# Optimization experiments

Measured on AMD Instinct MI355X. Metric: run time of the kernel, lower is better.

Reference implementation:

```python
import jax, jax.numpy as jnp
import numpy as np

B, D_IN, T = 8, 1024, 2048
CODEBOOK_SIZE, CODEBOOK_DIM = 8192, 8
EPS = 1e-12  # F.normalize default eps


def _l2_normalize(x, axis=-1):
    # matches torch F.normalize: x / max(||x||_2, eps)
    n = jnp.sqrt(jnp.sum(x * x, axis=axis, keepdims=True))
    return x / jnp.maximum(n, EPS)


def setup_inputs() -> dict:
    key = jax.random.key(0)
    k_z, k_wi, k_bi, k_wo, k_bo, k_cb = jax.random.split(key, 6)
    z = jax.random.normal(k_z, (B, D_IN, T), dtype=jnp.float32)
    # weight_norm(Conv1d) is a reparameterization; the effective weight is a
    # plain [out, in] matrix for a kernel_size=1 conv.
    w_in = jax.random.normal(k_wi, (CODEBOOK_DIM, D_IN), dtype=jnp.float32) * (1.0 / np.sqrt(D_IN))
    b_in = jax.random.normal(k_bi, (CODEBOOK_DIM,), dtype=jnp.float32) * 0.01
    w_out = jax.random.normal(k_wo, (D_IN, CODEBOOK_DIM), dtype=jnp.float32) * (1.0 / np.sqrt(CODEBOOK_DIM))
    b_out = jax.random.normal(k_bo, (D_IN,), dtype=jnp.float32) * 0.01
    codebook = jax.random.normal(k_cb, (CODEBOOK_SIZE, CODEBOOK_DIM), dtype=jnp.float32)
    return {"z": z, "w_in": w_in, "b_in": b_in, "w_out": w_out, "b_out": b_out, "codebook": codebook}


def reference(z, w_in, b_in, w_out, b_out, codebook):
    b, _, t = z.shape
    # in_project: 1x1 conv == matmul over channel dim
    z_e = jnp.einsum('od,bdt->bot', w_in, z) + b_in[None, :, None]  # [B, cd, T]

    # decode_latents
    enc = z_e.transpose(0, 2, 1).reshape(b * t, CODEBOOK_DIM)  # (b t) d
    enc_n = _l2_normalize(enc, axis=1)
    cb_n = _l2_normalize(codebook, axis=1)
    # dist = ||e||^2 - 2 e @ c^T + ||c||^2  (materializes [B*T, K] as original)
    dist = (jnp.sum(enc_n * enc_n, axis=1, keepdims=True)
            - 2.0 * (enc_n @ cb_n.T)
            + jnp.sum(cb_n * cb_n, axis=1)[None, :])
    indices = jnp.argmax(-dist, axis=1).reshape(b, t)  # [B, T] int
    # decode_code uses the UNnormalized codebook
    z_q = codebook[indices].transpose(0, 2, 1)  # [B, cd, T]

    # straight-through estimator
    z_q_st = z_e + jax.lax.stop_gradient(z_q - z_e)
    out = jnp.einsum('od,bdt->bot', w_out, z_q_st) + b_out[None, :, None]  # [B, D, T]

    commit_loss = jnp.zeros((b,), dtype=z.dtype)
    codebook_loss = jnp.zeros((b,), dtype=z.dtype)
    return (out, commit_loss, codebook_loss, indices, z_e)
```

## Files before the change

### kernel.cpp

```cpp
#include <hip/hip_runtime.h>
#include <math.h>

static constexpr int Bq  = 8;
static constexpr int DIN = 1024;
static constexpr int TTT = 2048;
static constexpr int KCB = 8192;

static constexpr int NCH = 64;
static constexpr int CPC = 128;

static constexpr size_t OUT_OFS  = 0;
static constexpr size_t LOSS_OFS = (size_t)Bq * DIN * TTT;
static constexpr size_t IDX_OFS  = LOSS_OFS + 16;
static constexpr size_t ZE_OFS   = IDX_OFS + (size_t)Bq * TTT;

static constexpr size_t WS_CBN  = 0;
static constexpr size_t WS_C2   = 65536;
static constexpr size_t WS_WT   = 73728;
static constexpr size_t WS_ENC  = 81920;
static constexpr size_t WS_PART = 212992;
static constexpr size_t WS_IDXI = WS_PART + (size_t)2 * NCH * 16384;

__global__ __launch_bounds__(256) void k0_prep(
    const float* __restrict__ w_in, const float* __restrict__ codebook,
    float* __restrict__ ws, float* __restrict__ out)
{
  int tid = blockIdx.x * 256 + threadIdx.x;
  if (tid < KCB) {
    const float4* cp = (const float4*)(codebook + (size_t)tid * 8);
    float4 a = cp[0], b = cp[1];
    float v[8] = {a.x, a.y, a.z, a.w, b.x, b.y, b.z, b.w};
    float n2 = 0.f;
#pragma unroll
    for (int o = 0; o < 8; o++) n2 = fmaf(v[o], v[o], n2);
    float dn = fmaxf(sqrtf(n2), 1e-12f);
    float u[8];
    float s2 = 0.f;
#pragma unroll
    for (int o = 0; o < 8; o++) { u[o] = v[o] / dn; s2 = fmaf(u[o], u[o], s2); }
    float4* wp = (float4*)(ws + WS_CBN + (size_t)tid * 8);
    wp[0] = make_float4(u[0], u[1], u[2], u[3]);
    wp[1] = make_float4(u[4], u[5], u[6], u[7]);
    ws[WS_C2 + tid] = 0.5f * s2;
  } else if (tid < KCB + DIN) {
    int d = tid - KCB;
#pragma unroll
    for (int o = 0; o < 8; o++) ws[WS_WT + (size_t)d * 8 + o] = w_in[(size_t)o * DIN + d];
  } else if (tid < KCB + DIN + 16) {
    out[LOSS_OFS + (tid - KCB - DIN)] = 0.f;
  }
}

__global__ __launch_bounds__(512) void k1_proj_in(
    const float* __restrict__ z, const float* __restrict__ b_in,
    float* __restrict__ ws, float* __restrict__ out)
{
  __shared__ __align__(16) float lds[16384];
  int tid = threadIdx.x;
  int bx = blockIdx.x;
  int b = bx >> 5;
  int t0 = (bx & 31) << 6;
  {
    const float4* src = (const float4*)(ws + WS_WT);
    float4* dst = (float4*)lds;
#pragma unroll
    for (int i = 0; i < 4; i++) dst[tid + 512 * i] = src[tid + 512 * i];
  }
  __syncthreads();
  int tt = tid & 15;
  int dg = tid >> 4;
  const float* zb = z + (size_t)b * DIN * TTT + t0 + (tt << 2);
  float4 acc[8];
#pragma unroll
  for (int o = 0; o < 8; o++) acc[o] = make_float4(0.f, 0.f, 0.f, 0.f);
  int dbase = dg << 5;
  const float4* wl = (const float4*)lds;
#pragma unroll 8
  for (int i = 0; i < 32; i++) {
    int d = dbase + i;
    float4 zv = *(const float4*)(zb + (size_t)d * TTT);
    float4 w0 = wl[d * 2 + 0];
    float4 w1 = wl[d * 2 + 1];
#define ACC1(o, wsc)                                    \
    acc[o].x = fmaf(wsc, zv.x, acc[o].x);               \
    acc[o].y = fmaf(wsc, zv.y, acc[o].y);               \
    acc[o].z = fmaf(wsc, zv.z, acc[o].z);               \
    acc[o].w = fmaf(wsc, zv.w, acc[o].w);
    ACC1(0, w0.x) ACC1(1, w0.y) ACC1(2, w0.z) ACC1(3, w0.w)
    ACC1(4, w1.x) ACC1(5, w1.y) ACC1(6, w1.z) ACC1(7, w1.w)
#undef ACC1
  }
  __syncthreads();
  {
    float4* pl = (float4*)lds;
#pragma unroll
    for (int o = 0; o < 8; o++) pl[dg * 128 + o * 16 + tt] = acc[o];
  }
  __syncthreads();
  int o = tid >> 6;
  int t = tid & 63;
  float s = 0.f;
#pragma unroll
  for (int g = 0; g < 32; g++) s += lds[g * 512 + o * 64 + t];
  s += b_in[o];
  out[ZE_OFS + ((size_t)b * 8 + o) * TTT + t0 + t] = s;
  ws[WS_ENC + ((size_t)(b * TTT + t0 + t)) * 8 + o] = s;
}

__global__ __launch_bounds__(256) void k2_scan(float* __restrict__ ws)
{
  __shared__ __align__(16) float4 scb[CPC * 2];
  __shared__ float sch[CPC];
  int tid = threadIdx.x;
  int rb = blockIdx.x >> 6;
  int ch = blockIdx.x & 63;
  int k0 = ch << 7;
  if (tid < CPC) {
    const float4* src = (const float4*)(ws + WS_CBN + (size_t)(k0 + tid) * 8);
    scb[tid * 2]     = src[0];
    scb[tid * 2 + 1] = src[1];
    sch[tid] = ws[WS_C2 + k0 + tid];
  }
  int rbase = (rb << 11) + tid;

#define DECL_ROW(j) float4 m##j##a, m##j##b; float b##j = 3.4e38f; int i##j = 0;
  DECL_ROW(0) DECL_ROW(1) DECL_ROW(2) DECL_ROW(3)
  DECL_ROW(4) DECL_ROW(5) DECL_ROW(6) DECL_ROW(7)
#undef DECL_ROW

#define LOAD_ROW(j) {                                                         \
    int r = rbase + (j << 8);                                                 \
    const float4* ep = (const float4*)(ws + WS_ENC + (size_t)r * 8);          \
    float4 a = ep[0], c = ep[1];                                              \
    float n2 = 0.f;                                                           \
    n2 = fmaf(a.x, a.x, n2); n2 = fmaf(a.y, a.y, n2);                         \
    n2 = fmaf(a.z, a.z, n2); n2 = fmaf(a.w, a.w, n2);                         \
    n2 = fmaf(c.x, c.x, n2); n2 = fmaf(c.y, c.y, n2);                         \
    n2 = fmaf(c.z, c.z, n2); n2 = fmaf(c.w, c.w, n2);                         \
    float dn = fmaxf(sqrtf(n2), 1e-12f);                                      \
    m##j##a.x = -(a.x / dn); m##j##a.y = -(a.y / dn);                         \
    m##j##a.z = -(a.z / dn); m##j##a.w = -(a.w / dn);                         \
    m##j##b.x = -(c.x / dn); m##j##b.y = -(c.y / dn);                         \
    m##j##b.z = -(c.z / dn); m##j##b.w = -(c.w / dn); }
  LOAD_ROW(0) LOAD_ROW(1) LOAD_ROW(2) LOAD_ROW(3)
  LOAD_ROW(4) LOAD_ROW(5) LOAD_ROW(6) LOAD_ROW(7)
#undef LOAD_ROW

  __syncthreads();
#pragma unroll 4
  for (int k = 0; k < CPC; k++) {
    float4 c0 = scb[2 * k];
    float4 c1 = scb[2 * k + 1];
    float cc = sch[k];
    int kk = k0 + k;
#define STEP(j) {                                                             \
    float s = cc;                                                             \
    s = fmaf(m##j##a.x, c0.x, s); s = fmaf(m##j##a.y, c0.y, s);               \
    s = fmaf(m##j##a.z, c0.z, s); s = fmaf(m##j##a.w, c0.w, s);               \
    s = fmaf(m##j##b.x, c1.x, s); s = fmaf(m##j##b.y, c1.y, s);               \
    s = fmaf(m##j##b.z, c1.z, s); s = fmaf(m##j##b.w, c1.w, s);               \
    if (s < b##j) { b##j = s; i##j = kk; } }
    STEP(0) STEP(1) STEP(2) STEP(3) STEP(4) STEP(5) STEP(6) STEP(7)
#undef STEP
  }
  float2* part = (float2*)(ws + WS_PART);
#define STORE_ROW(j) \
  part[(size_t)ch * 16384 + rbase + (j << 8)] = make_float2(b##j, __int_as_float(i##j));
  STORE_ROW(0) STORE_ROW(1) STORE_ROW(2) STORE_ROW(3)
  STORE_ROW(4) STORE_ROW(5) STORE_ROW(6) STORE_ROW(7)
#undef STORE_ROW
}

__global__ __launch_bounds__(256) void k2b_reduce(float* __restrict__ ws, float* __restrict__ out)
{
  int r = blockIdx.x * 256 + threadIdx.x;
  const float2* part = (const float2*)(ws + WS_PART);
  float best = 3.4e38f;
  int bi = 0;
#pragma unroll 8
  for (int ch = 0; ch < NCH; ch++) {
    float2 p = part[(size_t)ch * 16384 + r];
    if (p.x < best) { best = p.x; bi = __float_as_int(p.y); }
  }
  out[IDX_OFS + r] = (float)bi;
  ((int*)(ws + WS_IDXI))[r] = bi;
}

__global__ __launch_bounds__(256) void k3_proj_out(
    const float* __restrict__ codebook, const float* __restrict__ w_out,
    const float* __restrict__ b_out, const float* __restrict__ ws,
    float* __restrict__ out)
{
  int bx = blockIdx.x;
  int b = bx >> 7;
  int th = (bx >> 6) & 1;
  int dt = bx & 63;
  int tid = threadIdx.x;
  int t = (th << 10) + (tid << 2);
  const int* idxp = (const int*)(ws + WS_IDXI);
  int4 id = *(const int4*)(idxp + b * TTT + t);
  const float4* cbp = (const float4*)codebook;
  float4 c00 = cbp[(size_t)id.x * 2], c01 = cbp[(size_t)id.x * 2 + 1];
  float4 c10 = cbp[(size_t)id.y * 2], c11 = cbp[(size_t)id.y * 2 + 1];
  float4 c20 = cbp[(size_t)id.z * 2], c21 = cbp[(size_t)id.z * 2 + 1];
  float4 c30 = cbp[(size_t)id.w * 2], c31 = cbp[(size_t)id.w * 2 + 1];
  int d0 = dt << 4;
#pragma unroll 4
  for (int dd = 0; dd < 16; dd++) {
    int d = d0 + dd;
    const float* wr = w_out + (size_t)d * 8;
    float w0 = wr[0], w1 = wr[1], w2 = wr[2], w3 = wr[3];
    float w4 = wr[4], w5 = wr[5], w6 = wr[6], w7 = wr[7];
    float bb = b_out[d];
#define DOT8(lo, hi)                                                          \
    fmaf(w7, hi.w, fmaf(w6, hi.z, fmaf(w5, hi.y, fmaf(w4, hi.x,              \
    fmaf(w3, lo.w, fmaf(w2, lo.z, fmaf(w1, lo.y, fmaf(w0, lo.x, bb))))))))
    float4 r;
    r.x = DOT8(c00, c01);
    r.y = DOT8(c10, c11);
    r.z = DOT8(c20, c21);
    r.w = DOT8(c30, c31);
#undef DOT8
    *(float4*)(out + OUT_OFS + ((size_t)b * DIN + d) * TTT + t) = r;
  }
}

extern "C" void kernel_launch(void* const* d_in, const int* in_sizes, int n_in,
                              void* d_out, int out_size, void* d_ws, size_t ws_size,
                              hipStream_t stream) {
  const float* z        = (const float*)d_in[0];
  const float* w_in     = (const float*)d_in[1];
  const float* b_in     = (const float*)d_in[2];
  const float* w_out    = (const float*)d_in[3];
  const float* b_out    = (const float*)d_in[4];
  const float* codebook = (const float*)d_in[5];
  float* out = (float*)d_out;
  float* ws  = (float*)d_ws;

  k0_prep<<<dim3(37), dim3(256), 0, stream>>>(w_in, codebook, ws, out);
  k1_proj_in<<<dim3(256), dim3(512), 0, stream>>>(z, b_in, ws, out);
  k2_scan<<<dim3(512), dim3(256), 0, stream>>>(ws);
  k2b_reduce<<<dim3(64), dim3(256), 0, stream>>>(ws, out);
  k3_proj_out<<<dim3(1024), dim3(256), 0, stream>>>(codebook, w_out, b_out, ws, out);
}
```

Baseline: 196.1 us.

## Track only min score in scan, recover argmin index by rescanning winning chunk

The codebook scan now keeps only the minimum distance per row, using v_min3 to fold two candidates per step, and drops the per-candidate index tracking and compare/select. The reduce kernel finds the winning chunk and rescans its 128 entries to recover the index. Rows per thread drop from 8 to 4 and the grid doubles to 1024 blocks, which raises parallelism. The cost is an extra 128-entry rescan per row, and tie-breaking must still give the first index, which depends on the chunk rescan reproducing identical scores.

```diff
diff --git a/kernel.cpp b/kernel.cpp
--- a/kernel.cpp
+++ b/kernel.cpp
@@ -19,7 +19,32 @@
 static constexpr size_t WS_WT   = 73728;
 static constexpr size_t WS_ENC  = 81920;
 static constexpr size_t WS_PART = 212992;
-static constexpr size_t WS_IDXI = WS_PART + (size_t)2 * NCH * 16384;
+static constexpr size_t WS_IDXI = WS_PART + (size_t)NCH * 16384;
+
+__device__ __forceinline__ void load_enc_neg_norm(const float* __restrict__ ws,
+                                                  int r, float4& ma, float4& mb) {
+  const float4* ep = (const float4*)(ws + WS_ENC + (size_t)r * 8);
+  float4 a = ep[0], c = ep[1];
+  float n2 = 0.f;
+  n2 = fmaf(a.x, a.x, n2); n2 = fmaf(a.y, a.y, n2);
+  n2 = fmaf(a.z, a.z, n2); n2 = fmaf(a.w, a.w, n2);
+  n2 = fmaf(c.x, c.x, n2); n2 = fmaf(c.y, c.y, n2);
+  n2 = fmaf(c.z, c.z, n2); n2 = fmaf(c.w, c.w, n2);
+  float dn = fmaxf(sqrtf(n2), 1e-12f);
+  ma.x = -(a.x / dn); ma.y = -(a.y / dn);
+  ma.z = -(a.z / dn); ma.w = -(a.w / dn);
+  mb.x = -(c.x / dn); mb.y = -(c.y / dn);
+  mb.z = -(c.z / dn); mb.w = -(c.w / dn);
+}
+
+__device__ __forceinline__ float score8(const float4& ma, const float4& mb,
+                                        const float4& c0, const float4& c1, float cc) {
+  float s = fmaf(ma.x, c0.x, cc);
+  s = fmaf(ma.y, c0.y, s); s = fmaf(ma.z, c0.z, s); s = fmaf(ma.w, c0.w, s);
+  s = fmaf(mb.x, c1.x, s); s = fmaf(mb.y, c1.y, s);
+  s = fmaf(mb.z, c1.z, s); s = fmaf(mb.w, c1.w, s);
+  return s;
+}
 
 __global__ __launch_bounds__(256) void k0_prep(
     const float* __restrict__ w_in, const float* __restrict__ codebook,
@@ -121,66 +146,64 @@
     scb[tid * 2 + 1] = src[1];
     sch[tid] = ws[WS_C2 + k0 + tid];
   }
-  int rbase = (rb << 11) + tid;
-
-#define DECL_ROW(j) float4 m##j##a, m##j##b; float b##j = 3.4e38f; int i##j = 0;
-  DECL_ROW(0) DECL_ROW(1) DECL_ROW(2) DECL_ROW(3)
-  DECL_ROW(4) DECL_ROW(5) DECL_ROW(6) DECL_ROW(7)
-#undef DECL_ROW
-
-#define LOAD_ROW(j) {                                                         \
-    int r = rbase + (j << 8);                                                 \
-    const float4* ep = (const float4*)(ws + WS_ENC + (size_t)r * 8);          \
-    float4 a = ep[0], c = ep[1];                                              \
-    float n2 = 0.f;                                                           \
-    n2 = fmaf(a.x, a.x, n2); n2 = fmaf(a.y, a.y, n2);                         \
-    n2 = fmaf(a.z, a.z, n2); n2 = fmaf(a.w, a.w, n2);                         \
-    n2 = fmaf(c.x, c.x, n2); n2 = fmaf(c.y, c.y, n2);                         \
-    n2 = fmaf(c.z, c.z, n2); n2 = fmaf(c.w, c.w, n2);                         \
-    float dn = fmaxf(sqrtf(n2), 1e-12f);                                      \
-    m##j##a.x = -(a.x / dn); m##j##a.y = -(a.y / dn);                         \
-    m##j##a.z = -(a.z / dn); m##j##a.w = -(a.w / dn);                         \
-    m##j##b.x = -(c.x / dn); m##j##b.y = -(c.y / dn);                         \
-    m##j##b.z = -(c.z / dn); m##j##b.w = -(c.w / dn); }
-  LOAD_ROW(0) LOAD_ROW(1) LOAD_ROW(2) LOAD_ROW(3)
-  LOAD_ROW(4) LOAD_ROW(5) LOAD_ROW(6) LOAD_ROW(7)
-#undef LOAD_ROW
-
-  __syncthreads();
+  int rbase = (rb << 10) + tid;
+
+  float4 m0a, m0b, m1a, m1b, m2a, m2b, m3a, m3b;
+  load_enc_neg_norm(ws, rbase,       m0a, m0b);
+  load_enc_neg_norm(ws, rbase + 256, m1a, m1b);
+  load_enc_neg_norm(ws, rbase + 512, m2a, m2b);
+  load_enc_neg_norm(ws, rbase + 768, m3a, m3b);
+  float b0 = 3.4e38f, b1 = 3.4e38f, b2 = 3.4e38f, b3 = 3.4e38f;
+
+  __syncthreads();
+#pragma unroll 2
+  for (int k = 0; k < CPC; k += 2) {
+    float4 c00 = scb[2 * k + 0];
+    float4 c01 = scb[2 * k + 1];
+    float4 c10 = scb[2 * k + 2];
+    float4 c11 = scb[2 * k + 3];
+    float ca = sch[k];
+    float cb = sch[k + 1];
+#define STEP2(ma, mb, bj) {                                                   \
+    float s0 = score8(ma, mb, c00, c01, ca);                                  \
+    float s1 = score8(ma, mb, c10, c11, cb);                                  \
+    asm("v_min3_f32 %0, %1, %2, %3" : "=v"(bj) : "v"(bj), "v"(s0), "v"(s1)); }
+    STEP2(m0a, m0b, b0)
+    STEP2(m1a, m1b, b1)
+    STEP2(m2a, m2b, b2)
+    STEP2(m3a, m3b, b3)
+#undef STEP2
+  }
+  float* part = ws + WS_PART + (size_t)ch * 16384 + rbase;
+  part[0]   = b0;
+  part[256] = b1;
+  part[512] = b2;
+  part[768] = b3;
+}
+
+__global__ __launch_bounds__(256) void k2b_argmin(float* __restrict__ ws, float* __restrict__ out)
+{
+  int r = blockIdx.x * 256 + threadIdx.x;
+  const float* part = ws + WS_PART;
+  float m = 3.4e38f;
+  int cbest = 0;
+#pragma unroll 8
+  for (int ch = 0; ch < NCH; ch++) {
+    float p = part[(size_t)ch * 16384 + r];
+    if (p < m) { m = p; cbest = ch; }
+  }
+  float4 ma, mb;
+  load_enc_neg_norm(ws, r, ma, mb);
+  int base = cbest << 7;
+  float best = 3.4e38f;
+  int bi = 0;
 #pragma unroll 4
   for (int k = 0; k < CPC; k++) {
-    float4 c0 = scb[2 * k];
-    float4 c1 = scb[2 * k + 1];
-    float cc = sch[k];
-    int kk = k0 + k;
-#define STEP(j) {                                                             \
-    float s = cc;                                                             \
-    s = fmaf(m##j##a.x, c0.x, s); s = fmaf(m##j##a.y, c0.y, s);               \
-    s = fmaf(m##j##a.z, c0.z, s); s = fmaf(m##j##a.w, c0.w, s);               \
-    s = fmaf(m##j##b.x, c1.x, s); s = fmaf(m##j##b.y, c1.y, s);               \
-    s = fmaf(m##j##b.z, c1.z, s); s = fmaf(m##j##b.w, c1.w, s);               \
-    if (s < b##j) { b##j = s; i##j = kk; } }
-    STEP(0) STEP(1) STEP(2) STEP(3) STEP(4) STEP(5) STEP(6) STEP(7)
-#undef STEP
-  }
-  float2* part = (float2*)(ws + WS_PART);
-#define STORE_ROW(j) \
-  part[(size_t)ch * 16384 + rbase + (j << 8)] = make_float2(b##j, __int_as_float(i##j));
-  STORE_ROW(0) STORE_ROW(1) STORE_ROW(2) STORE_ROW(3)
-  STORE_ROW(4) STORE_ROW(5) STORE_ROW(6) STORE_ROW(7)
-#undef STORE_ROW
-}
-
-__global__ __launch_bounds__(256) void k2b_reduce(float* __restrict__ ws, float* __restrict__ out)
-{
-  int r = blockIdx.x * 256 + threadIdx.x;
-  const float2* part = (const float2*)(ws + WS_PART);
-  float best = 3.4e38f;
-  int bi = 0;
-#pragma unroll 8
-  for (int ch = 0; ch < NCH; ch++) {
-    float2 p = part[(size_t)ch * 16384 + r];
-    if (p.x < best) { best = p.x; bi = __float_as_int(p.y); }
+    const float4* cp = (const float4*)(ws + WS_CBN + (size_t)(base + k) * 8);
+    float4 c0 = cp[0], c1 = cp[1];
+    float cc = ws[WS_C2 + base + k];
+    float s = score8(ma, mb, c0, c1, cc);
+    if (s < best) { best = s; bi = base + k; }
   }
   out[IDX_OFS + r] = (float)bi;
   ((int*)(ws + WS_IDXI))[r] = bi;
@@ -239,7 +262,7 @@
 
   k0_prep<<<dim3(37), dim3(256), 0, stream>>>(w_in, codebook, ws, out);
   k1_proj_in<<<dim3(256), dim3(512), 0, stream>>>(z, b_in, ws, out);
-  k2_scan<<<dim3(512), dim3(256), 0, stream>>>(ws);
-  k2b_reduce<<<dim3(64), dim3(256), 0, stream>>>(ws, out);
+  k2_scan<<<dim3(1024), dim3(256), 0, stream>>>(ws);
+  k2b_argmin<<<dim3(64), dim3(256), 0, stream>>>(ws, out);
   k3_proj_out<<<dim3(1024), dim3(256), 0, stream>>>(codebook, w_out, b_out, ws, out);
 }
```

Measured after the change: 207.3 us. +5.7%, slower.
